# Kernel optimization log

Hardware: AMD Instinct MI355X
Metric: run time of the kernel (lower is better)

The kernel has to match this reference:

```python
import jax, jax.numpy as jnp
import numpy as np

N_NODES = 50000


def _gcn_conv(x, src, dst, W, b, num_nodes):
    """PyG GCNConv: out = D^{-1/2}(A+I)D^{-1/2} (x @ W) + b, self-loops added."""
    h = x @ W  # [N, out]
    # degrees over edges incl. self-loops (src/dst already include self-loops)
    ones = jnp.ones(src.shape[0], dtype=h.dtype)
    deg = jax.ops.segment_sum(ones, dst, num_segments=num_nodes)
    dinv = jnp.where(deg > 0, jax.lax.rsqrt(deg), 0.0)
    norm = dinv[src] * dinv[dst]  # [E]
    msgs = h[src] * norm[:, None]  # [E, out] gather (memory-bound)
    out = jax.ops.segment_sum(msgs, dst, num_segments=num_nodes)
    return out + b


def setup_inputs() -> dict:
    key = jax.random.key(0)
    ks = jax.random.split(key, 8)
    in_c, h2, h1, out_c = 256, 256, 128, 128
    x = jax.random.normal(ks[0], (N_NODES, in_c), dtype=jnp.float32)
    edge_index = jax.random.randint(ks[1], (2, 800000), 0, N_NODES, dtype=jnp.int64)
    def glorot(k, fi, fo):
        s = float(np.sqrt(6.0 / (fi + fo)))
        return jax.random.uniform(k, (fi, fo), jnp.float32, -s, s)
    return {
        "x": x,
        "edge_index": edge_index,
        "W1": glorot(ks[2], in_c, h2), "b1": jnp.zeros((h2,), jnp.float32),
        "W2": glorot(ks[3], h2, h1), "b2": jnp.zeros((h1,), jnp.float32),
        "W3": glorot(ks[4], h1, out_c), "b3": jnp.zeros((out_c,), jnp.float32),
    }


def reference(x, edge_index, W1, b1, W2, b2, W3, b3):
    n = x.shape[0]
    loops = jnp.arange(n, dtype=edge_index.dtype)
    src = jnp.concatenate([edge_index[0], loops])
    dst = jnp.concatenate([edge_index[1], loops])
    # dropout is a no-op in eval mode (training=False)
    h1 = jax.nn.relu(_gcn_conv(x, src, dst, W1, b1, n))
    h2 = jax.nn.relu(_gcn_conv(h1, src, dst, W2, b2, n))
    h3 = jax.nn.relu(_gcn_conv(h2, src, dst, W3, b3, n))
    return jnp.concatenate([h1, h2, h3], axis=1)
```

## Files before the change

### kernel.cpp

```cpp
#include <hip/hip_runtime.h>

typedef __attribute__((ext_vector_type(8))) short bfrag8;
typedef __attribute__((ext_vector_type(4))) float f32x4v;

__device__ inline short f2bf(float f) {
    unsigned u = __builtin_bit_cast(unsigned, f);
    u = (u + 0x7FFFu + ((u >> 16) & 1u)) >> 16;
    return (short)u;
}
__device__ inline float bf2f(short s) {
    unsigned u = ((unsigned)(unsigned short)s) << 16;
    return __builtin_bit_cast(float, u);
}
__device__ inline int pack2(short lo, short hi) {
    return (int)(((unsigned)(unsigned short)lo) | (((unsigned)(unsigned short)hi) << 16));
}


__global__ void deg_count_kernel(const int* __restrict__ dst, int E, int* __restrict__ deg) {
    int e = blockIdx.x * blockDim.x + threadIdx.x;
    if (e < E) atomicAdd(&deg[dst[e]], 1);
}

__global__ void block_sum_kernel(const int* __restrict__ deg, int n, int* __restrict__ bsums) {
    int i = blockIdx.x * 256 + threadIdx.x;
    int v = (i < n) ? deg[i] : 0;
#pragma unroll
    for (int off = 32; off > 0; off >>= 1) v += __shfl_down(v, off);
    __shared__ int wsum[4];
    int lane = threadIdx.x & 63, w = threadIdx.x >> 6;
    if (lane == 0) wsum[w] = v;
    __syncthreads();
    if (threadIdx.x == 0) bsums[blockIdx.x] = wsum[0] + wsum[1] + wsum[2] + wsum[3];
}

__global__ void scan_bsums_kernel(int* __restrict__ bsums, int B, int* __restrict__ offs, int n) {
    __shared__ int s[256];
    int tid = threadIdx.x;
    int v = (tid < B) ? bsums[tid] : 0;
    s[tid] = v;
    __syncthreads();
    for (int off = 1; off < 256; off <<= 1) {
        int t = (tid >= off) ? s[tid - off] : 0;
        __syncthreads();
        s[tid] += t;
        __syncthreads();
    }
    if (tid < B) bsums[tid] = (tid == 0) ? 0 : s[tid - 1];
    if (tid == 0) offs[n] = s[255];
}

__global__ void scan_final_kernel(const int* __restrict__ deg, int n,
                                  const int* __restrict__ bsums,
                                  int* __restrict__ offs, int* __restrict__ cursor,
                                  float* __restrict__ dinv) {
    __shared__ int s[256];
    int tid = threadIdx.x;
    int i = blockIdx.x * 256 + tid;
    int v = (i < n) ? deg[i] : 0;
    s[tid] = v;
    __syncthreads();
    for (int off = 1; off < 256; off <<= 1) {
        int t = (tid >= off) ? s[tid - off] : 0;
        __syncthreads();
        s[tid] += t;
        __syncthreads();
    }
    if (i < n) {
        int excl = s[tid] - v + bsums[blockIdx.x];
        offs[i] = excl;
        cursor[i] = excl;
        dinv[i] = rsqrtf((float)(v + 1));
    }
}

__global__ void csr_fill_kernel(const int* __restrict__ src, const int* __restrict__ dst, int E,
                                int* __restrict__ cursor, int* __restrict__ csr) {
    int e = blockIdx.x * blockDim.x + threadIdx.x;
    if (e < E) {
        int d = dst[e];
        int p = atomicAdd(&cursor[d], 1);
        csr[p] = src[e];
    }
}


__global__ void wt_kernel(const float* __restrict__ W, short* __restrict__ Wt,
                          int K, int logN) {
    int i = blockIdx.x * blockDim.x + threadIdx.x;
    int total = K << logN;
    if (i < total) {
        int k = i >> logN;
        int n = i & ((1 << logN) - 1);
        Wt[(size_t)n * K + k] = f2bf(W[i]);
    }
}


__global__ void x2b_kernel(const float* __restrict__ x, short* __restrict__ xb, int total8) {
    int i = blockIdx.x * blockDim.x + threadIdx.x;
    if (i < total8) {
        const float4* p = (const float4*)(x + (size_t)i * 8);
        float4 v0 = p[0], v1 = p[1];
        int4 w = make_int4(pack2(f2bf(v0.x), f2bf(v0.y)), pack2(f2bf(v0.z), f2bf(v0.w)),
                           pack2(f2bf(v1.x), f2bf(v1.y)), pack2(f2bf(v1.z), f2bf(v1.w)));
        *(int4*)(xb + (size_t)i * 8) = w;
    }
}


template<int K>
__global__ __launch_bounds__(256, 2) void gemm_skinny_kernel(
        const short* __restrict__ A,
        const short* __restrict__ Bt,
        const float* __restrict__ dinv,
        short* __restrict__ Tout, int ldt) {
    constexpr int BSTR = K + 8;
    __shared__ short Bs[64 * BSTR];

    const int tid = threadIdx.x;
    const int lane = tid & 63;
    const int wid = tid >> 6;
    const int l15 = lane & 15;
    const int quad = lane >> 4;
    const int q8 = quad * 8;
    const int bn = blockIdx.y * 64;
    const int row0 = blockIdx.x * 256 + wid * 64;

    {
        constexpr int TOT16 = 64 * K / 8;
#pragma unroll
        for (int i = tid; i < TOT16; i += 256) {
            int r = i / (K / 8);
            int c = (i % (K / 8)) * 8;
            *(int4*)&Bs[r * BSTR + c] = *(const int4*)&Bt[(size_t)(bn + r) * K + c];
        }
    }
    __syncthreads();

    f32x4v acc[4][4];
#pragma unroll
    for (int i = 0; i < 4; ++i)
#pragma unroll
        for (int j = 0; j < 4; ++j) acc[i][j] = (f32x4v){0.f, 0.f, 0.f, 0.f};

    const short* aBase = A + (size_t)(row0 + l15) * K + q8;

#pragma unroll
    for (int ks = 0; ks < K / 32; ++ks) {
        bfrag8 af[4], bf[4];
#pragma unroll
        for (int mt = 0; mt < 4; ++mt)
            af[mt] = *(const bfrag8*)(aBase + (size_t)mt * 16 * K + ks * 32);
#pragma unroll
        for (int nt = 0; nt < 4; ++nt)
            bf[nt] = *(const bfrag8*)&Bs[(nt * 16 + l15) * BSTR + ks * 32 + q8];
#pragma unroll
        for (int mt = 0; mt < 4; ++mt)
#pragma unroll
            for (int nt = 0; nt < 4; ++nt)
                acc[mt][nt] = __builtin_amdgcn_mfma_f32_16x16x32_bf16(af[mt], bf[nt], acc[mt][nt], 0, 0, 0);
    }

#pragma unroll
    for (int mt = 0; mt < 4; ++mt) {
#pragma unroll
        for (int r = 0; r < 4; ++r) {
            int grow = row0 + mt * 16 + quad * 4 + r;
            float di = dinv[grow];
            short* outp = Tout + (size_t)grow * ldt + bn + l15;
#pragma unroll
            for (int nt = 0; nt < 4; ++nt)
                outp[nt * 16] = f2bf(acc[mt][nt][r] * di);
        }
    }
}


template<int C, bool WB>
__global__ __launch_bounds__(256) void agg_kernel(
        const short* __restrict__ hn, const float* __restrict__ dinv,
        const int* __restrict__ offs, const int* __restrict__ csr,
        const float* __restrict__ bias, float* __restrict__ out,
        short* __restrict__ hb, int coloff, int n) {
    constexpr int V = C / 64;
    int node = blockIdx.x * 4 + (threadIdx.x >> 6);
    if (node >= n) return;
    int lane = threadIdx.x & 63;
    const short* base = hn + lane * V;

    float acc[V];
#pragma unroll
    for (int v = 0; v < V; ++v) acc[v] = 0.f;

    int beg = offs[node], end = offs[node + 1];
    int e = beg;
    if (V == 4) {
        for (; e + 8 <= end; e += 8) {
            short4 r[8];
#pragma unroll
            for (int j = 0; j < 8; ++j)
                r[j] = *(const short4*)(base + (size_t)csr[e + j] * C);
#pragma unroll
            for (int j = 0; j < 8; ++j) {
                acc[0] += bf2f(r[j].x); acc[1] += bf2f(r[j].y);
                acc[2] += bf2f(r[j].z); acc[3] += bf2f(r[j].w);
            }
        }
        for (; e < end; ++e) {
            short4 a = *(const short4*)(base + (size_t)csr[e] * C);
            acc[0] += bf2f(a.x); acc[1] += bf2f(a.y); acc[2] += bf2f(a.z); acc[3] += bf2f(a.w);
        }
        short4 a = *(const short4*)(base + (size_t)node * C);
        acc[0] += bf2f(a.x); acc[1] += bf2f(a.y); acc[2] += bf2f(a.z); acc[3] += bf2f(a.w);
    } else {
        for (; e + 8 <= end; e += 8) {
            short2 r[8];
#pragma unroll
            for (int j = 0; j < 8; ++j)
                r[j] = *(const short2*)(base + (size_t)csr[e + j] * C);
#pragma unroll
            for (int j = 0; j < 8; ++j) {
                acc[0] += bf2f(r[j].x); acc[1] += bf2f(r[j].y);
            }
        }
        for (; e < end; ++e) {
            short2 a = *(const short2*)(base + (size_t)csr[e] * C);
            acc[0] += bf2f(a.x); acc[1] += bf2f(a.y);
        }
        short2 a = *(const short2*)(base + (size_t)node * C);
        acc[0] += bf2f(a.x); acc[1] += bf2f(a.y);
    }

    float di = dinv[node];
    float res[V];
#pragma unroll
    for (int v = 0; v < V; ++v)
        res[v] = fmaxf(fmaf(di, acc[v], bias[lane * V + v]), 0.f);

    float* op = out + (size_t)node * 512 + coloff + lane * V;
    if (V == 4) {
        *(float4*)op = make_float4(res[0], res[1], res[2], res[3]);
        if (WB) {
            int2 w = make_int2(pack2(f2bf(res[0]), f2bf(res[1])), pack2(f2bf(res[2]), f2bf(res[3])));
            *(int2*)(hb + (size_t)node * C + lane * V) = w;
        }
    } else {
        *(float2*)op = make_float2(res[0], res[1]);
        if (WB) {
            *(int*)(hb + (size_t)node * C + lane * V) = pack2(f2bf(res[0]), f2bf(res[1]));
        }
    }
}


extern "C" void kernel_launch(void* const* d_in, const int* in_sizes, int n_in,
                              void* d_out, int out_size, void* d_ws, size_t ws_size,
                              hipStream_t stream) {
    const float* x  = (const float*)d_in[0];
    const int*   ei = (const int*)d_in[1];
    const float* W1 = (const float*)d_in[2];
    const float* b1 = (const float*)d_in[3];
    const float* W2 = (const float*)d_in[4];
    const float* b2 = (const float*)d_in[5];
    const float* W3 = (const float*)d_in[6];
    const float* b3 = (const float*)d_in[7];

    const int IN_C = 256, H2 = 256, H1 = 128, OUT_C = 128;
    int n = in_sizes[0] / IN_C;
    int E = in_sizes[1] / 2;
    const int* src = ei;
    const int* dst = ei + E;

    int sb = (n + 255) / 256;
    int npad = sb * 256;

    char* ws = (char*)d_ws;
    auto carve = [&](size_t bytes) { char* p = ws; ws += (bytes + 255) & ~(size_t)255; return p; };
    int*   deg    = (int*)  carve((size_t)n * 4);
    int*   offs   = (int*)  carve(((size_t)n + 1) * 4);
    int*   cursor = (int*)  carve((size_t)n * 4);
    float* dinv   = (float*)carve((size_t)npad * 4);
    int*   csr    = (int*)  carve((size_t)E * 4);
    int*   bsums  = (int*)  carve(256 * 4);
    short* Wt1    = (short*)carve((size_t)IN_C * H2 * 2);
    short* Wt2    = (short*)carve((size_t)H2 * H1 * 2);
    short* Wt3    = (short*)carve((size_t)H1 * OUT_C * 2);
    short* t      = (short*)carve((size_t)npad * 256 * 2);
    short* inb    = (short*)carve((size_t)npad * 256 * 2);

    float* out = (float*)d_out;
    int nblk = (n + 255) / 256;

    hipMemsetAsync(deg, 0, (size_t)n * sizeof(int), stream);
    deg_count_kernel<<<(E + 255) / 256, 256, 0, stream>>>(dst, E, deg);
    block_sum_kernel<<<nblk, 256, 0, stream>>>(deg, n, bsums);
    scan_bsums_kernel<<<1, 256, 0, stream>>>(bsums, nblk, offs, n);
    scan_final_kernel<<<nblk, 256, 0, stream>>>(deg, n, bsums, offs, cursor, dinv);
    csr_fill_kernel<<<(E + 255) / 256, 256, 0, stream>>>(src, dst, E, cursor, csr);

    wt_kernel<<<(IN_C * H2 + 255) / 256, 256, 0, stream>>>(W1, Wt1, IN_C, 8);
    wt_kernel<<<(H2 * H1 + 255) / 256, 256, 0, stream>>>(W2, Wt2, H2, 7);
    wt_kernel<<<(H1 * OUT_C + 255) / 256, 256, 0, stream>>>(W3, Wt3, H1, 7);

    int total8 = n * IN_C / 8;
    x2b_kernel<<<(total8 + 255) / 256, 256, 0, stream>>>(x, inb, total8);

    gemm_skinny_kernel<256><<<dim3(sb, H2 / 64), 256, 0, stream>>>(inb, Wt1, dinv, t, H2);
    agg_kernel<256, true><<<(n + 3) / 4, 256, 0, stream>>>(t, dinv, offs, csr, b1, out, inb, 0, n);

    gemm_skinny_kernel<256><<<dim3(sb, H1 / 64), 256, 0, stream>>>(inb, Wt2, dinv, t, H1);
    agg_kernel<128, true><<<(n + 3) / 4, 256, 0, stream>>>(t, dinv, offs, csr, b2, out, inb, H2, n);

    gemm_skinny_kernel<128><<<dim3(sb, OUT_C / 64), 256, 0, stream>>>(inb, Wt3, dinv, t, OUT_C);
    agg_kernel<128, false><<<(n + 3) / 4, 256, 0, stream>>>(t, dinv, offs, csr, b3, out, nullptr, H2 + H1, n);
}
```

Baseline: 443.1 us.

## Split aggregation into column slices with edge-parallel lanes and shuffle reduction

The aggregation kernel now splits each node's feature row into 32-column slices handled by separate blocks. Within a wavefront, four lane groups each gather a different neighbor's 2-element chunk, and the partial sums are combined with cross-lane shuffles. This targets gather latency and memory-level parallelism on power-law-free random graphs, at the cost of more blocks, repeated CSR index reads per slice, and narrower 4-byte loads. The three weight-transpose launches are also merged into one kernel to cut launch overhead.

```diff
diff --git a/kernel.cpp b/kernel.cpp
--- a/kernel.cpp
+++ b/kernel.cpp
@@ -85,14 +85,21 @@
 }
 
 
-__global__ void wt_kernel(const float* __restrict__ W, short* __restrict__ Wt,
-                          int K, int logN) {
+__global__ void prep_w_kernel(const float* __restrict__ W1, short* __restrict__ Wt1,
+                              const float* __restrict__ W2, short* __restrict__ Wt2,
+                              const float* __restrict__ W3, short* __restrict__ Wt3) {
     int i = blockIdx.x * blockDim.x + threadIdx.x;
-    int total = K << logN;
-    if (i < total) {
-        int k = i >> logN;
-        int n = i & ((1 << logN) - 1);
-        Wt[(size_t)n * K + k] = f2bf(W[i]);
+    if (i < 65536) {
+        int k = i >> 8, n = i & 255;
+        Wt1[n * 256 + k] = f2bf(W1[i]);
+    } else if (i < 65536 + 32768) {
+        int j = i - 65536;
+        int k = j >> 7, n = j & 127;
+        Wt2[n * 256 + k] = f2bf(W2[j]);
+    } else {
+        int j = i - 65536 - 32768;
+        int k = j >> 7, n = j & 127;
+        Wt3[n * 128 + k] = f2bf(W3[j]);
     }
 }
 
@@ -177,79 +184,63 @@
 }
 
 
-template<int C, bool WB>
-__global__ __launch_bounds__(256) void agg_kernel(
+template<int C, int NSLICE, bool WB>
+__global__ __launch_bounds__(256) void agg_sliced_kernel(
         const short* __restrict__ hn, const float* __restrict__ dinv,
         const int* __restrict__ offs, const int* __restrict__ csr,
         const float* __restrict__ bias, float* __restrict__ out,
         short* __restrict__ hb, int coloff, int n) {
-    constexpr int V = C / 64;
-    int node = blockIdx.x * 4 + (threadIdx.x >> 6);
+    const int wid = threadIdx.x >> 6;
+    const int slice = blockIdx.x % NSLICE;
+    const int node = (blockIdx.x / NSLICE) * 4 + wid;
     if (node >= n) return;
-    int lane = threadIdx.x & 63;
-    const short* base = hn + lane * V;
-
-    float acc[V];
-#pragma unroll
-    for (int v = 0; v < V; ++v) acc[v] = 0.f;
-
+    const int lane = threadIdx.x & 63;
+    const int eg = lane >> 4;
+    const int cl = lane & 15;
+    const int c0 = slice * 32 + cl * 2;
+    const short* base = hn + c0;
+
+    float ax = 0.f, ay = 0.f;
     int beg = offs[node], end = offs[node + 1];
     int e = beg;
-    if (V == 4) {
-        for (; e + 8 <= end; e += 8) {
-            short4 r[8];
-#pragma unroll
-            for (int j = 0; j < 8; ++j)
-                r[j] = *(const short4*)(base + (size_t)csr[e + j] * C);
-#pragma unroll
-            for (int j = 0; j < 8; ++j) {
-                acc[0] += bf2f(r[j].x); acc[1] += bf2f(r[j].y);
-                acc[2] += bf2f(r[j].z); acc[3] += bf2f(r[j].w);
-            }
-        }
-        for (; e < end; ++e) {
-            short4 a = *(const short4*)(base + (size_t)csr[e] * C);
-            acc[0] += bf2f(a.x); acc[1] += bf2f(a.y); acc[2] += bf2f(a.z); acc[3] += bf2f(a.w);
-        }
-        short4 a = *(const short4*)(base + (size_t)node * C);
-        acc[0] += bf2f(a.x); acc[1] += bf2f(a.y); acc[2] += bf2f(a.z); acc[3] += bf2f(a.w);
-    } else {
-        for (; e + 8 <= end; e += 8) {
-            short2 r[8];
-#pragma unroll
-            for (int j = 0; j < 8; ++j)
-                r[j] = *(const short2*)(base + (size_t)csr[e + j] * C);
-#pragma unroll
-            for (int j = 0; j < 8; ++j) {
-                acc[0] += bf2f(r[j].x); acc[1] += bf2f(r[j].y);
-            }
-        }
-        for (; e < end; ++e) {
-            short2 a = *(const short2*)(base + (size_t)csr[e] * C);
-            acc[0] += bf2f(a.x); acc[1] += bf2f(a.y);
-        }
+    for (; e + 8 <= end; e += 8) {
+        int s0 = csr[e + eg];
+        int s1 = csr[e + 4 + eg];
+        short2 a = *(const short2*)(base + (size_t)s0 * C);
+        short2 b = *(const short2*)(base + (size_t)s1 * C);
+        ax += bf2f(a.x) + bf2f(b.x);
+        ay += bf2f(a.y) + bf2f(b.y);
+    }
+    if (e + 4 <= end) {
+        int s0 = csr[e + eg];
+        short2 a = *(const short2*)(base + (size_t)s0 * C);
+        ax += bf2f(a.x);
+        ay += bf2f(a.y);
+        e += 4;
+    }
+    int rem = end - e;
+    if (eg < rem) {
+        int s0 = csr[e + eg];
+        short2 a = *(const short2*)(base + (size_t)s0 * C);
+        ax += bf2f(a.x);
+        ay += bf2f(a.y);
+    }
+    if (eg == 0) {
         short2 a = *(const short2*)(base + (size_t)node * C);
-        acc[0] += bf2f(a.x); acc[1] += bf2f(a.y);
-    }
-
-    float di = dinv[node];
-    float res[V];
-#pragma unroll
-    for (int v = 0; v < V; ++v)
-        res[v] = fmaxf(fmaf(di, acc[v], bias[lane * V + v]), 0.f);
-
-    float* op = out + (size_t)node * 512 + coloff + lane * V;
-    if (V == 4) {
-        *(float4*)op = make_float4(res[0], res[1], res[2], res[3]);
-        if (WB) {
-            int2 w = make_int2(pack2(f2bf(res[0]), f2bf(res[1])), pack2(f2bf(res[2]), f2bf(res[3])));
-            *(int2*)(hb + (size_t)node * C + lane * V) = w;
-        }
-    } else {
-        *(float2*)op = make_float2(res[0], res[1]);
-        if (WB) {
-            *(int*)(hb + (size_t)node * C + lane * V) = pack2(f2bf(res[0]), f2bf(res[1]));
-        }
+        ax += bf2f(a.x);
+        ay += bf2f(a.y);
+    }
+
+    ax += __shfl_xor(ax, 16); ax += __shfl_xor(ax, 32);
+    ay += __shfl_xor(ay, 16); ay += __shfl_xor(ay, 32);
+
+    if (eg == 0) {
+        float di = dinv[node];
+        float rx = fmaxf(fmaf(di, ax, bias[c0 + 0]), 0.f);
+        float ry = fmaxf(fmaf(di, ay, bias[c0 + 1]), 0.f);
+        *(float2*)(out + (size_t)node * 512 + coloff + c0) = make_float2(rx, ry);
+        if (WB)
+            *(int*)(hb + (size_t)node * C + c0) = pack2(f2bf(rx), f2bf(ry));
     }
 }
 
@@ -291,6 +282,7 @@
 
     float* out = (float*)d_out;
     int nblk = (n + 255) / 256;
+    int ng4 = (n + 3) / 4;
 
     hipMemsetAsync(deg, 0, (size_t)n * sizeof(int), stream);
     deg_count_kernel<<<(E + 255) / 256, 256, 0, stream>>>(dst, E, deg);
@@ -299,19 +291,17 @@
     scan_final_kernel<<<nblk, 256, 0, stream>>>(deg, n, bsums, offs, cursor, dinv);
     csr_fill_kernel<<<(E + 255) / 256, 256, 0, stream>>>(src, dst, E, cursor, csr);
 
-    wt_kernel<<<(IN_C * H2 + 255) / 256, 256, 0, stream>>>(W1, Wt1, IN_C, 8);
-    wt_kernel<<<(H2 * H1 + 255) / 256, 256, 0, stream>>>(W2, Wt2, H2, 7);
-    wt_kernel<<<(H1 * OUT_C + 255) / 256, 256, 0, stream>>>(W3, Wt3, H1, 7);
+    prep_w_kernel<<<(65536 + 32768 + 16384 + 255) / 256, 256, 0, stream>>>(W1, Wt1, W2, Wt2, W3, Wt3);
 
     int total8 = n * IN_C / 8;
     x2b_kernel<<<(total8 + 255) / 256, 256, 0, stream>>>(x, inb, total8);
 
     gemm_skinny_kernel<256><<<dim3(sb, H2 / 64), 256, 0, stream>>>(inb, Wt1, dinv, t, H2);
-    agg_kernel<256, true><<<(n + 3) / 4, 256, 0, stream>>>(t, dinv, offs, csr, b1, out, inb, 0, n);
+    agg_sliced_kernel<256, 8, true><<<ng4 * 8, 256, 0, stream>>>(t, dinv, offs, csr, b1, out, inb, 0, n);
 
     gemm_skinny_kernel<256><<<dim3(sb, H1 / 64), 256, 0, stream>>>(inb, Wt2, dinv, t, H1);
-    agg_kernel<128, true><<<(n + 3) / 4, 256, 0, stream>>>(t, dinv, offs, csr, b2, out, inb, H2, n);
+    agg_sliced_kernel<128, 4, true><<<ng4 * 4, 256, 0, stream>>>(t, dinv, offs, csr, b2, out, inb, H2, n);
 
     gemm_skinny_kernel<128><<<dim3(sb, OUT_C / 64), 256, 0, stream>>>(inb, Wt3, dinv, t, OUT_C);
-    agg_kernel<128, false><<<(n + 3) / 4, 256, 0, stream>>>(t, dinv, offs, csr, b3, out, nullptr, H2 + H1, n);
-}
+    agg_sliced_kernel<128, 4, false><<<ng4 * 4, 256, 0, stream>>>(t, dinv, offs, csr, b3, out, nullptr, H2 + H1, n);
+}
```

After: 635.1 us. 1.43x slower.
